# Kernel tuning notes

Hardware: AMD Instinct MI355X
Metric: run time of the kernel (lower is better)

Reference implementation:

```python
import jax, jax.numpy as jnp
import numpy as np
from jax import lax

T, N, F, H, E = 8, 20000, 128, 256, 320000
LEAK = 0.9


def setup_inputs() -> dict:
    key = jax.random.key(0)
    k = jax.random.split(key, 7)
    x = jax.random.normal(k[0], (T, N, F), dtype=jnp.float32)
    edge_index = jax.random.randint(k[1], (2, E), 0, N, dtype=jnp.int32)
    # reservoir weights, scaled ~1/sqrt(fan_in) so tanh stays in its active range
    w_in0 = jax.random.normal(k[2], (H, F), dtype=jnp.float32) / jnp.sqrt(F)
    w_rec0 = jax.random.normal(k[3], (H, H), dtype=jnp.float32) / jnp.sqrt(H)
    w_in1 = jax.random.normal(k[4], (H, H), dtype=jnp.float32) / jnp.sqrt(H)
    w_rec1 = jax.random.normal(k[5], (H, H), dtype=jnp.float32) / jnp.sqrt(H)
    leakage = jnp.array(LEAK, dtype=jnp.float32)
    return {"x": x, "edge_index": edge_index, "w_in0": w_in0, "w_rec0": w_rec0,
            "w_in1": w_in1, "w_rec1": w_rec1, "leakage": leakage}


def reference(x, edge_index, w_in0, w_rec0, w_in1, w_rec1, leakage):
    # DynamicGraphReservoir with 2 ReservoirConvLayers, fixed graph over time,
    # zero initial states, no pooling, fully=False, return_sequences=False.
    src, dst = edge_index[0], edge_index[1]
    num_nodes = x.shape[1]

    def layer(w_in, w_rec, inp, state):
        # neighbour aggregation: sum_{(j->i) in E} state[j]   (scatter-add)
        agg = jax.ops.segment_sum(state[src], dst, num_segments=num_nodes)
        return leakage * jnp.tanh(inp @ w_in.T + agg @ w_rec.T) + (1.0 - leakage) * state

    def step(states, xt):
        s0, s1 = states
        s0 = layer(w_in0, w_rec0, xt, s0)   # layer 0 consumes input signal
        s1 = layer(w_in1, w_rec1, s0, s1)   # layer 1 consumes layer-0 state
        return (s0, s1), None

    init = (jnp.zeros((num_nodes, w_rec0.shape[0]), x.dtype),
            jnp.zeros((num_nodes, w_rec1.shape[0]), x.dtype))
    (s0, s1), _ = lax.scan(step, init, x)
    return s1  # final-layer final state: (nodes, hidden)
```

## Files before the change

### kernel.cpp

```cpp
#include <hip/hip_runtime.h>
#include <math.h>

#define T_STEPS 8
#define N_NODES 20000
#define F_IN    128
#define H_DIM   256
#define E_EDGES 320000

typedef __attribute__((ext_vector_type(8))) short short8;
typedef __attribute__((ext_vector_type(4))) float f32x4;

__device__ __forceinline__ void split2(float v, unsigned short& h, unsigned short& l) {
    unsigned vi = __float_as_uint(v);
    h = (unsigned short)(vi >> 16);
    float hf = __uint_as_float(vi & 0xffff0000u);
    l = (unsigned short)(__float_as_uint(v - hf) >> 16);
}


__global__ void count_kernel(const int* __restrict__ dst, int* __restrict__ counts, int E) {
    int e = blockIdx.x * blockDim.x + threadIdx.x;
    if (e < E) atomicAdd(&counts[dst[e]], 1);
}

__global__ void scan_kernel(const int* __restrict__ counts, int* __restrict__ row_ptr,
                            int* __restrict__ cursors, int n) {
    __shared__ int buf[1024];
    __shared__ int carry_s;
    int tid = threadIdx.x;
    if (tid == 0) carry_s = 0;
    __syncthreads();
    for (int base = 0; base < n; base += 1024) {
        int i = base + tid;
        int v = (i < n) ? counts[i] : 0;
        buf[tid] = v;
        __syncthreads();
        for (int off = 1; off < 1024; off <<= 1) {
            int t = (tid >= off) ? buf[tid - off] : 0;
            __syncthreads();
            buf[tid] += t;
            __syncthreads();
        }
        int incl = buf[tid];
        int carry = carry_s;
        if (i < n) {
            int ex = carry + incl - v;
            row_ptr[i] = ex;
            cursors[i] = ex;
        }
        __syncthreads();
        if (tid == 1023) carry_s = carry + incl;
        __syncthreads();
    }
    if (tid == 0) row_ptr[n] = carry_s;
}

__global__ void fill_kernel(const int* __restrict__ src, const int* __restrict__ dst,
                            int* __restrict__ cursors, int* __restrict__ col, int E) {
    int e = blockIdx.x * blockDim.x + threadIdx.x;
    if (e < E) {
        int d = dst[e];
        int p = atomicAdd(&cursors[d], 1);
        col[p] = src[e];
    }
}


__global__ void cvt_frag(const float* __restrict__ W, int K,
                         unsigned short* __restrict__ fh, unsigned short* __restrict__ fl) {
    int g = blockIdx.x * 256 + threadIdx.x;
    int KP32 = K >> 5;
    int total = (H_DIM / 16) * KP32 * 64;
    if (g >= total) return;
    int lane = g & 63;
    int kp = (g >> 6) % KP32;
    int rt = g / (KP32 << 6);
    int r = rt * 16 + (lane & 15);
    int c = kp * 32 + (lane >> 4) * 8;
    const float* p = W + (size_t)r * K + c;
    short8 h, l;
    #pragma unroll
    for (int j = 0; j < 8; ++j) {
        unsigned short hh, ll;
        split2(p[j], hh, ll);
        h[j] = (short)hh; l[j] = (short)ll;
    }
    *(short8*)(fh + (size_t)g * 8) = h;
    *(short8*)(fl + (size_t)g * 8) = l;
}


__global__ __launch_bounds__(256) void fused_update(
        const float* __restrict__ A1, int K1,
        const float* __restrict__ s_prev,
        const unsigned short* __restrict__ B1h, const unsigned short* __restrict__ B1l,
        const unsigned short* __restrict__ B2h, const unsigned short* __restrict__ B2l,
        float* __restrict__ s_new,
        const int* __restrict__ row_ptr, const int* __restrict__ col,
        const float* __restrict__ leak_ptr, int do_gather) {
    __shared__ float aggs[32][260];
    const int tid = threadIdx.x;
    const int lane = tid & 63, w = tid >> 6;
    const int fr = lane & 15, fq = lane >> 4;
    const int m0 = blockIdx.x * 32;
    const int wn = w * 64;
    const int rtbase = w * 4;

    if (do_gather) {
        const float4* s4 = (const float4*)s_prev;
        #pragma unroll 1
        for (int i = 0; i < 8; ++i) {
            int r = w * 8 + i;
            int beg = row_ptr[m0 + r], end = row_ptr[m0 + r + 1];
            float4 a0 = {0,0,0,0}, a1 = {0,0,0,0}, a2 = {0,0,0,0}, a3 = {0,0,0,0};
            float4 a4 = {0,0,0,0}, a5 = {0,0,0,0}, a6 = {0,0,0,0}, a7 = {0,0,0,0};
            int j = beg;
            for (; j + 7 < end; j += 8) {
                float4 v0 = s4[(size_t)col[j    ] * 64 + lane];
                float4 v1 = s4[(size_t)col[j + 1] * 64 + lane];
                float4 v2 = s4[(size_t)col[j + 2] * 64 + lane];
                float4 v3 = s4[(size_t)col[j + 3] * 64 + lane];
                float4 v4 = s4[(size_t)col[j + 4] * 64 + lane];
                float4 v5 = s4[(size_t)col[j + 5] * 64 + lane];
                float4 v6 = s4[(size_t)col[j + 6] * 64 + lane];
                float4 v7 = s4[(size_t)col[j + 7] * 64 + lane];
                a0.x += v0.x; a0.y += v0.y; a0.z += v0.z; a0.w += v0.w;
                a1.x += v1.x; a1.y += v1.y; a1.z += v1.z; a1.w += v1.w;
                a2.x += v2.x; a2.y += v2.y; a2.z += v2.z; a2.w += v2.w;
                a3.x += v3.x; a3.y += v3.y; a3.z += v3.z; a3.w += v3.w;
                a4.x += v4.x; a4.y += v4.y; a4.z += v4.z; a4.w += v4.w;
                a5.x += v5.x; a5.y += v5.y; a5.z += v5.z; a5.w += v5.w;
                a6.x += v6.x; a6.y += v6.y; a6.z += v6.z; a6.w += v6.w;
                a7.x += v7.x; a7.y += v7.y; a7.z += v7.z; a7.w += v7.w;
            }
            for (; j + 3 < end; j += 4) {
                float4 v0 = s4[(size_t)col[j    ] * 64 + lane];
                float4 v1 = s4[(size_t)col[j + 1] * 64 + lane];
                float4 v2 = s4[(size_t)col[j + 2] * 64 + lane];
                float4 v3 = s4[(size_t)col[j + 3] * 64 + lane];
                a0.x += v0.x; a0.y += v0.y; a0.z += v0.z; a0.w += v0.w;
                a1.x += v1.x; a1.y += v1.y; a1.z += v1.z; a1.w += v1.w;
                a2.x += v2.x; a2.y += v2.y; a2.z += v2.z; a2.w += v2.w;
                a3.x += v3.x; a3.y += v3.y; a3.z += v3.z; a3.w += v3.w;
            }
            for (; j < end; ++j) {
                float4 v = s4[(size_t)col[j] * 64 + lane];
                a0.x += v.x; a0.y += v.y; a0.z += v.z; a0.w += v.w;
            }
            float4 t;
            t.x = ((a0.x + a1.x) + (a2.x + a3.x)) + ((a4.x + a5.x) + (a6.x + a7.x));
            t.y = ((a0.y + a1.y) + (a2.y + a3.y)) + ((a4.y + a5.y) + (a6.y + a7.y));
            t.z = ((a0.z + a1.z) + (a2.z + a3.z)) + ((a4.z + a5.z) + (a6.z + a7.z));
            t.w = ((a0.w + a1.w) + (a2.w + a3.w)) + ((a4.w + a5.w) + (a6.w + a7.w));
            *(float4*)&aggs[r][lane * 4] = t;
        }
    }

    f32x4 acc[2][4];
    #pragma unroll
    for (int mi = 0; mi < 2; ++mi)
        #pragma unroll
        for (int nt = 0; nt < 4; ++nt)
            acc[mi][nt] = (f32x4){0.f, 0.f, 0.f, 0.f};

    {
        const int KP32 = K1 >> 5;
        #pragma unroll 1
        for (int kp = 0; kp < KP32; ++kp) {
            short8 ah[2], al[2];
            #pragma unroll
            for (int mi = 0; mi < 2; ++mi) {
                const float* ap = A1 + (size_t)(m0 + mi * 16 + fr) * K1 + kp * 32 + fq * 8;
                float4 v0 = *(const float4*)ap;
                float4 v1 = *(const float4*)(ap + 4);
                unsigned short h, l;
                split2(v0.x, h, l); ah[mi][0] = (short)h; al[mi][0] = (short)l;
                split2(v0.y, h, l); ah[mi][1] = (short)h; al[mi][1] = (short)l;
                split2(v0.z, h, l); ah[mi][2] = (short)h; al[mi][2] = (short)l;
                split2(v0.w, h, l); ah[mi][3] = (short)h; al[mi][3] = (short)l;
                split2(v1.x, h, l); ah[mi][4] = (short)h; al[mi][4] = (short)l;
                split2(v1.y, h, l); ah[mi][5] = (short)h; al[mi][5] = (short)l;
                split2(v1.z, h, l); ah[mi][6] = (short)h; al[mi][6] = (short)l;
                split2(v1.w, h, l); ah[mi][7] = (short)h; al[mi][7] = (short)l;
            }
            short8 bh[4], bl[4];
            #pragma unroll
            for (int nt = 0; nt < 4; ++nt) {
                size_t off = ((size_t)((rtbase + nt) * KP32 + kp) * 64 + lane) * 8;
                bh[nt] = *(const short8*)(B1h + off);
                bl[nt] = *(const short8*)(B1l + off);
            }
            #pragma unroll
            for (int mi = 0; mi < 2; ++mi)
                #pragma unroll
                for (int nt = 0; nt < 4; ++nt) {
                    f32x4 c = acc[mi][nt];
                    c = __builtin_amdgcn_mfma_f32_16x16x32_bf16(ah[mi], bh[nt], c, 0, 0, 0);
                    c = __builtin_amdgcn_mfma_f32_16x16x32_bf16(al[mi], bh[nt], c, 0, 0, 0);
                    c = __builtin_amdgcn_mfma_f32_16x16x32_bf16(ah[mi], bl[nt], c, 0, 0, 0);
                    acc[mi][nt] = c;
                }
        }
    }

    if (B2h) {
        __syncthreads();
        #pragma unroll 1
        for (int kp = 0; kp < 8; ++kp) {
            short8 ah[2], al[2];
            #pragma unroll
            for (int mi = 0; mi < 2; ++mi) {
                const float* ap = &aggs[mi * 16 + fr][kp * 32 + fq * 8];
                float4 v0 = *(const float4*)ap;
                float4 v1 = *(const float4*)(ap + 4);
                unsigned short h, l;
                split2(v0.x, h, l); ah[mi][0] = (short)h; al[mi][0] = (short)l;
                split2(v0.y, h, l); ah[mi][1] = (short)h; al[mi][1] = (short)l;
                split2(v0.z, h, l); ah[mi][2] = (short)h; al[mi][2] = (short)l;
                split2(v0.w, h, l); ah[mi][3] = (short)h; al[mi][3] = (short)l;
                split2(v1.x, h, l); ah[mi][4] = (short)h; al[mi][4] = (short)l;
                split2(v1.y, h, l); ah[mi][5] = (short)h; al[mi][5] = (short)l;
                split2(v1.z, h, l); ah[mi][6] = (short)h; al[mi][6] = (short)l;
                split2(v1.w, h, l); ah[mi][7] = (short)h; al[mi][7] = (short)l;
            }
            short8 bh[4], bl[4];
            #pragma unroll
            for (int nt = 0; nt < 4; ++nt) {
                size_t off = ((size_t)((rtbase + nt) * 8 + kp) * 64 + lane) * 8;
                bh[nt] = *(const short8*)(B2h + off);
                bl[nt] = *(const short8*)(B2l + off);
            }
            #pragma unroll
            for (int mi = 0; mi < 2; ++mi)
                #pragma unroll
                for (int nt = 0; nt < 4; ++nt) {
                    f32x4 c = acc[mi][nt];
                    c = __builtin_amdgcn_mfma_f32_16x16x32_bf16(ah[mi], bh[nt], c, 0, 0, 0);
                    c = __builtin_amdgcn_mfma_f32_16x16x32_bf16(al[mi], bh[nt], c, 0, 0, 0);
                    c = __builtin_amdgcn_mfma_f32_16x16x32_bf16(ah[mi], bl[nt], c, 0, 0, 0);
                    acc[mi][nt] = c;
                }
        }
    }

    const float leak = leak_ptr[0], il = 1.0f - leak;
    #pragma unroll
    for (int mi = 0; mi < 2; ++mi)
        #pragma unroll
        for (int r = 0; r < 4; ++r) {
            int m = m0 + mi * 16 + fq * 4 + r;
            #pragma unroll
            for (int nt = 0; nt < 4; ++nt) {
                int n = wn + nt * 16 + fr;
                size_t idx = (size_t)m * H_DIM + n;
                float old = s_prev[idx];
                float pre = acc[mi][nt][r];
                float e = __expf(2.0f * pre);
                float th = 1.0f - 2.0f / (e + 1.0f);
                s_new[idx] = leak * th + il * old;
            }
        }
}


extern "C" void kernel_launch(void* const* d_in, const int* in_sizes, int n_in,
                              void* d_out, int out_size, void* d_ws, size_t ws_size,
                              hipStream_t stream) {
    const float* x        = (const float*)d_in[0];
    const int*   edge     = (const int*)d_in[1];
    const float* w_in0    = (const float*)d_in[2];
    const float* w_rec0   = (const float*)d_in[3];
    const float* w_in1    = (const float*)d_in[4];
    const float* w_rec1   = (const float*)d_in[5];
    const float* leak_ptr = (const float*)d_in[6];

    const int* src = edge;
    const int* dst = edge + E_EDGES;

    char* ws = (char*)d_ws;
    size_t off = 0;
    auto alloc = [&](size_t bytes) -> char* {
        char* p = ws + off;
        off += (bytes + 255) & ~(size_t)255;
        return p;
    };
    const size_t state_bytes = (size_t)N_NODES * H_DIM * sizeof(float);
    float* s0b[2]; float* s1b[2];
    s0b[0] = (float*)alloc(state_bytes);
    s0b[1] = (float*)alloc(state_bytes);
    s1b[0] = (float*)d_out;
    s1b[1] = (float*)alloc(state_bytes);
    unsigned short* w0h  = (unsigned short*)alloc(256 * 128 * 2);
    unsigned short* w0l  = (unsigned short*)alloc(256 * 128 * 2);
    unsigned short* wr0h = (unsigned short*)alloc(256 * 256 * 2);
    unsigned short* wr0l = (unsigned short*)alloc(256 * 256 * 2);
    unsigned short* w1h  = (unsigned short*)alloc(256 * 256 * 2);
    unsigned short* w1l  = (unsigned short*)alloc(256 * 256 * 2);
    unsigned short* wr1h = (unsigned short*)alloc(256 * 256 * 2);
    unsigned short* wr1l = (unsigned short*)alloc(256 * 256 * 2);
    int* row_ptr = (int*)alloc((N_NODES + 1) * sizeof(int));
    int* cursors = (int*)alloc(N_NODES * sizeof(int));
    int* counts  = (int*)alloc(N_NODES * sizeof(int));
    int* col     = (int*)alloc((size_t)E_EDGES * sizeof(int));

    hipMemsetAsync(s0b[0], 0, state_bytes, stream);
    hipMemsetAsync(s1b[0], 0, state_bytes, stream);
    hipMemsetAsync(counts, 0, N_NODES * sizeof(int), stream);

    cvt_frag<<<16, 256, 0, stream>>>(w_in0, F_IN, w0h, w0l);
    cvt_frag<<<32, 256, 0, stream>>>(w_rec0, H_DIM, wr0h, wr0l);
    cvt_frag<<<32, 256, 0, stream>>>(w_in1, H_DIM, w1h, w1l);
    cvt_frag<<<32, 256, 0, stream>>>(w_rec1, H_DIM, wr1h, wr1l);

    count_kernel<<<(E_EDGES + 255) / 256, 256, 0, stream>>>(dst, counts, E_EDGES);
    scan_kernel<<<1, 1024, 0, stream>>>(counts, row_ptr, cursors, N_NODES);
    fill_kernel<<<(E_EDGES + 255) / 256, 256, 0, stream>>>(src, dst, cursors, col, E_EDGES);

    dim3 ugrid(N_NODES / 32);

    for (int t = 0; t < T_STEPS; ++t) {
        const float* xt = x + (size_t)t * N_NODES * F_IN;
        int rd = t & 1, wr = rd ^ 1;
        int dg = (t > 0) ? 1 : 0;
        fused_update<<<ugrid, 256, 0, stream>>>(
            xt, F_IN, s0b[rd],
            w0h, w0l, dg ? wr0h : nullptr, dg ? wr0l : nullptr,
            s0b[wr], row_ptr, col, leak_ptr, dg);
        fused_update<<<ugrid, 256, 0, stream>>>(
            s0b[wr], H_DIM, s1b[rd],
            w1h, w1l, dg ? wr1h : nullptr, dg ? wr1l : nullptr,
            s1b[wr], row_ptr, col, leak_ptr, dg);
    }
}
```

Baseline: 1.172 ms.

## Skew layer-1 step t with layer-0 step t+1 into one merged launch

Layer 1 at step t and layer 0 at step t+1 both read only s0 at step t, so they are independent. This change runs them in a single kernel whose blocks alternate between the two tasks, which halves the launches in the time loop and doubles the blocks per launch. The aim is to cut launch overhead and tail idle time while keeping the per-block work unchanged. The risk is in the buffer ping-pong indexing across the skewed schedule, and in two working sets competing for cache at once.

```diff
diff --git a/kernel.cpp b/kernel.cpp
--- a/kernel.cpp
+++ b/kernel.cpp
@@ -90,19 +90,18 @@
 }
 
 
-__global__ __launch_bounds__(256) void fused_update(
+__device__ __forceinline__ void update_body(
         const float* __restrict__ A1, int K1,
         const float* __restrict__ s_prev,
         const unsigned short* __restrict__ B1h, const unsigned short* __restrict__ B1l,
         const unsigned short* __restrict__ B2h, const unsigned short* __restrict__ B2l,
         float* __restrict__ s_new,
         const int* __restrict__ row_ptr, const int* __restrict__ col,
-        const float* __restrict__ leak_ptr, int do_gather) {
-    __shared__ float aggs[32][260];
+        const float* __restrict__ leak_ptr, int do_gather,
+        int m0, float (*aggs)[260]) {
     const int tid = threadIdx.x;
     const int lane = tid & 63, w = tid >> 6;
     const int fr = lane & 15, fq = lane >> 4;
-    const int m0 = blockIdx.x * 32;
     const int wn = w * 64;
     const int rtbase = w * 4;
 
@@ -263,6 +262,48 @@
 }
 
 
+__global__ __launch_bounds__(256) void fused_update(
+        const float* __restrict__ A1, int K1,
+        const float* __restrict__ s_prev,
+        const unsigned short* __restrict__ B1h, const unsigned short* __restrict__ B1l,
+        const unsigned short* __restrict__ B2h, const unsigned short* __restrict__ B2l,
+        float* __restrict__ s_new,
+        const int* __restrict__ row_ptr, const int* __restrict__ col,
+        const float* __restrict__ leak_ptr, int do_gather) {
+    __shared__ float aggs[32][260];
+    update_body(A1, K1, s_prev, B1h, B1l, B2h, B2l, s_new,
+                row_ptr, col, leak_ptr, do_gather, blockIdx.x * 32, aggs);
+}
+
+
+__global__ __launch_bounds__(256) void fused_update2(
+        const float* __restrict__ A1a, int K1a, const float* __restrict__ spa,
+        const unsigned short* __restrict__ B1ha, const unsigned short* __restrict__ B1la,
+        const unsigned short* __restrict__ B2ha, const unsigned short* __restrict__ B2la,
+        float* __restrict__ sna, int dga,
+        const float* __restrict__ A1b, int K1b, const float* __restrict__ spb,
+        const unsigned short* __restrict__ B1hb, const unsigned short* __restrict__ B1lb,
+        const unsigned short* __restrict__ B2hb, const unsigned short* __restrict__ B2lb,
+        float* __restrict__ snb, int dgb,
+        const int* __restrict__ row_ptr, const int* __restrict__ col,
+        const float* __restrict__ leak_ptr) {
+    __shared__ float aggs[32][260];
+    const int task = blockIdx.x & 1;
+    const int m0 = (blockIdx.x >> 1) * 32;
+    const float* A1 = task ? A1b : A1a;
+    const int K1 = task ? K1b : K1a;
+    const float* sp = task ? spb : spa;
+    const unsigned short* B1h = task ? B1hb : B1ha;
+    const unsigned short* B1l = task ? B1lb : B1la;
+    const unsigned short* B2h = task ? B2hb : B2ha;
+    const unsigned short* B2l = task ? B2lb : B2la;
+    float* sn = task ? snb : sna;
+    const int dg = task ? dgb : dga;
+    update_body(A1, K1, sp, B1h, B1l, B2h, B2l, sn,
+                row_ptr, col, leak_ptr, dg, m0, aggs);
+}
+
+
 extern "C" void kernel_launch(void* const* d_in, const int* in_sizes, int n_in,
                               void* d_out, int out_size, void* d_ws, size_t ws_size,
                               hipStream_t stream) {
@@ -317,18 +358,33 @@
     fill_kernel<<<(E_EDGES + 255) / 256, 256, 0, stream>>>(src, dst, cursors, col, E_EDGES);
 
     dim3 ugrid(N_NODES / 32);
-
-    for (int t = 0; t < T_STEPS; ++t) {
-        const float* xt = x + (size_t)t * N_NODES * F_IN;
-        int rd = t & 1, wr = rd ^ 1;
-        int dg = (t > 0) ? 1 : 0;
-        fused_update<<<ugrid, 256, 0, stream>>>(
-            xt, F_IN, s0b[rd],
-            w0h, w0l, dg ? wr0h : nullptr, dg ? wr0l : nullptr,
-            s0b[wr], row_ptr, col, leak_ptr, dg);
-        fused_update<<<ugrid, 256, 0, stream>>>(
-            s0b[wr], H_DIM, s1b[rd],
-            w1h, w1l, dg ? wr1h : nullptr, dg ? wr1l : nullptr,
-            s1b[wr], row_ptr, col, leak_ptr, dg);
-    }
-}
+    dim3 ugrid2(2 * (N_NODES / 32));
+
+
+    fused_update<<<ugrid, 256, 0, stream>>>(
+        x, F_IN, s0b[0],
+        w0h, w0l, nullptr, nullptr,
+        s0b[1], row_ptr, col, leak_ptr, 0);
+
+    for (int m = 0; m < 7; ++m) {
+        const float* s0_cur = s0b[(m + 1) & 1];
+        float* s0_next      = s0b[m & 1];
+        const float* s1_rd  = s1b[m & 1];
+        float* s1_wr        = s1b[(m + 1) & 1];
+        const float* xt = x + (size_t)(m + 1) * N_NODES * F_IN;
+        int dg1 = (m > 0) ? 1 : 0;
+        fused_update2<<<ugrid2, 256, 0, stream>>>(
+            s0_cur, H_DIM, s1_rd,
+            w1h, w1l, dg1 ? wr1h : nullptr, dg1 ? wr1l : nullptr,
+            s1_wr, dg1,
+            xt, F_IN, s0_cur,
+            w0h, w0l, wr0h, wr0l,
+            s0_next, 1,
+            row_ptr, col, leak_ptr);
+    }
+
+    fused_update<<<ugrid, 256, 0, stream>>>(
+        s0b[0], H_DIM, s1b[1],
+        w1h, w1l, wr1h, wr1l,
+        s1b[0], row_ptr, col, leak_ptr, 1);
+}
```

Result: no change. 1.192 ms (+1.7%).

## Decouple neighbour gather from GEMM update and co-schedule it with the next layer

Applied to the files above, without the earlier changes.

Each state's neighbour aggregation now runs as a separate set of blocks in the kernel that produces the state's consumer-independent work. The aggregate is written to a global AGG buffer, so gather for the next layer overlaps with the current layer's GEMM update in one launch. The gather is re-split into 8 column chunks per 32-row group, with 8 lanes per edge slot and shuffle reductions. Column indices shrink to 16-bit. This trades the shared-memory aggregate and per-block serial gather for extra global traffic (writing and re-reading AGG) in exchange for better parallelism and overlap.

```diff
diff --git a/kernel.cpp b/kernel.cpp
--- a/kernel.cpp
+++ b/kernel.cpp
@@ -6,6 +6,9 @@
 #define F_IN    128
 #define H_DIM   256
 #define E_EDGES 320000
+
+#define G_UPD    625
+#define G_GATHER 5000
 
 typedef __attribute__((ext_vector_type(8))) short short8;
 typedef __attribute__((ext_vector_type(4))) float f32x4;
@@ -56,12 +59,12 @@
 }
 
 __global__ void fill_kernel(const int* __restrict__ src, const int* __restrict__ dst,
-                            int* __restrict__ cursors, int* __restrict__ col, int E) {
+                            int* __restrict__ cursors, unsigned short* __restrict__ col, int E) {
     int e = blockIdx.x * blockDim.x + threadIdx.x;
     if (e < E) {
         int d = dst[e];
         int p = atomicAdd(&cursors[d], 1);
-        col[p] = src[e];
+        col[p] = (unsigned short)src[e];
     }
 }
 
@@ -90,71 +93,62 @@
 }
 
 
-__global__ __launch_bounds__(256) void fused_update(
+__global__ __launch_bounds__(256) void step_kernel(
         const float* __restrict__ A1, int K1,
         const float* __restrict__ s_prev,
         const unsigned short* __restrict__ B1h, const unsigned short* __restrict__ B1l,
         const unsigned short* __restrict__ B2h, const unsigned short* __restrict__ B2l,
+        const float* __restrict__ AGGu,
         float* __restrict__ s_new,
-        const int* __restrict__ row_ptr, const int* __restrict__ col,
-        const float* __restrict__ leak_ptr, int do_gather) {
-    __shared__ float aggs[32][260];
+        const float* __restrict__ gsrc, float* __restrict__ gout, int do_gather,
+        const int* __restrict__ row_ptr, const unsigned short* __restrict__ col,
+        const float* __restrict__ leak_ptr) {
     const int tid = threadIdx.x;
     const int lane = tid & 63, w = tid >> 6;
+    const int upd_base = do_gather ? G_GATHER : 0;
+
+    if (blockIdx.x < (unsigned)upd_base) {
+        const int g = blockIdx.x;
+        const int chunk = g & 7;
+        const int nb = g >> 3;
+        const int slot = lane >> 3, comp = lane & 7;
+        const float4* src4 = (const float4*)gsrc + (size_t)chunk * 8 + comp;
+        #pragma unroll 1
+        for (int i = 0; i < 8; ++i) {
+            int r = nb * 32 + w * 8 + i;
+            int beg = row_ptr[r], end = row_ptr[r + 1];
+            float4 a = {0.f, 0.f, 0.f, 0.f};
+            int j = beg + slot;
+            for (; j + 8 < end; j += 16) {
+                int i0 = col[j];
+                int i1 = col[j + 8];
+                float4 v0 = src4[(size_t)i0 * 64];
+                float4 v1 = src4[(size_t)i1 * 64];
+                a.x += v0.x; a.y += v0.y; a.z += v0.z; a.w += v0.w;
+                a.x += v1.x; a.y += v1.y; a.z += v1.z; a.w += v1.w;
+            }
+            if (j < end) {
+                int i0 = col[j];
+                float4 v0 = src4[(size_t)i0 * 64];
+                a.x += v0.x; a.y += v0.y; a.z += v0.z; a.w += v0.w;
+            }
+            #pragma unroll
+            for (int m = 8; m < 64; m <<= 1) {
+                a.x += __shfl_xor(a.x, m);
+                a.y += __shfl_xor(a.y, m);
+                a.z += __shfl_xor(a.z, m);
+                a.w += __shfl_xor(a.w, m);
+            }
+            if (slot == 0)
+                *(float4*)(gout + (size_t)r * 256 + chunk * 32 + comp * 4) = a;
+        }
+        return;
+    }
+
+    const int m0 = (blockIdx.x - upd_base) * 32;
     const int fr = lane & 15, fq = lane >> 4;
-    const int m0 = blockIdx.x * 32;
     const int wn = w * 64;
     const int rtbase = w * 4;
-
-    if (do_gather) {
-        const float4* s4 = (const float4*)s_prev;
-        #pragma unroll 1
-        for (int i = 0; i < 8; ++i) {
-            int r = w * 8 + i;
-            int beg = row_ptr[m0 + r], end = row_ptr[m0 + r + 1];
-            float4 a0 = {0,0,0,0}, a1 = {0,0,0,0}, a2 = {0,0,0,0}, a3 = {0,0,0,0};
-            float4 a4 = {0,0,0,0}, a5 = {0,0,0,0}, a6 = {0,0,0,0}, a7 = {0,0,0,0};
-            int j = beg;
-            for (; j + 7 < end; j += 8) {
-                float4 v0 = s4[(size_t)col[j    ] * 64 + lane];
-                float4 v1 = s4[(size_t)col[j + 1] * 64 + lane];
-                float4 v2 = s4[(size_t)col[j + 2] * 64 + lane];
-                float4 v3 = s4[(size_t)col[j + 3] * 64 + lane];
-                float4 v4 = s4[(size_t)col[j + 4] * 64 + lane];
-                float4 v5 = s4[(size_t)col[j + 5] * 64 + lane];
-                float4 v6 = s4[(size_t)col[j + 6] * 64 + lane];
-                float4 v7 = s4[(size_t)col[j + 7] * 64 + lane];
-                a0.x += v0.x; a0.y += v0.y; a0.z += v0.z; a0.w += v0.w;
-                a1.x += v1.x; a1.y += v1.y; a1.z += v1.z; a1.w += v1.w;
-                a2.x += v2.x; a2.y += v2.y; a2.z += v2.z; a2.w += v2.w;
-                a3.x += v3.x; a3.y += v3.y; a3.z += v3.z; a3.w += v3.w;
-                a4.x += v4.x; a4.y += v4.y; a4.z += v4.z; a4.w += v4.w;
-                a5.x += v5.x; a5.y += v5.y; a5.z += v5.z; a5.w += v5.w;
-                a6.x += v6.x; a6.y += v6.y; a6.z += v6.z; a6.w += v6.w;
-                a7.x += v7.x; a7.y += v7.y; a7.z += v7.z; a7.w += v7.w;
-            }
-            for (; j + 3 < end; j += 4) {
-                float4 v0 = s4[(size_t)col[j    ] * 64 + lane];
-                float4 v1 = s4[(size_t)col[j + 1] * 64 + lane];
-                float4 v2 = s4[(size_t)col[j + 2] * 64 + lane];
-                float4 v3 = s4[(size_t)col[j + 3] * 64 + lane];
-                a0.x += v0.x; a0.y += v0.y; a0.z += v0.z; a0.w += v0.w;
-                a1.x += v1.x; a1.y += v1.y; a1.z += v1.z; a1.w += v1.w;
-                a2.x += v2.x; a2.y += v2.y; a2.z += v2.z; a2.w += v2.w;
-                a3.x += v3.x; a3.y += v3.y; a3.z += v3.z; a3.w += v3.w;
-            }
-            for (; j < end; ++j) {
-                float4 v = s4[(size_t)col[j] * 64 + lane];
-                a0.x += v.x; a0.y += v.y; a0.z += v.z; a0.w += v.w;
-            }
-            float4 t;
-            t.x = ((a0.x + a1.x) + (a2.x + a3.x)) + ((a4.x + a5.x) + (a6.x + a7.x));
-            t.y = ((a0.y + a1.y) + (a2.y + a3.y)) + ((a4.y + a5.y) + (a6.y + a7.y));
-            t.z = ((a0.z + a1.z) + (a2.z + a3.z)) + ((a4.z + a5.z) + (a6.z + a7.z));
-            t.w = ((a0.w + a1.w) + (a2.w + a3.w)) + ((a4.w + a5.w) + (a6.w + a7.w));
-            *(float4*)&aggs[r][lane * 4] = t;
-        }
-    }
 
     f32x4 acc[2][4];
     #pragma unroll
@@ -204,13 +198,12 @@
     }
 
     if (B2h) {
-        __syncthreads();
         #pragma unroll 1
         for (int kp = 0; kp < 8; ++kp) {
             short8 ah[2], al[2];
             #pragma unroll
             for (int mi = 0; mi < 2; ++mi) {
-                const float* ap = &aggs[mi * 16 + fr][kp * 32 + fq * 8];
+                const float* ap = AGGu + (size_t)(m0 + mi * 16 + fr) * H_DIM + kp * 32 + fq * 8;
                 float4 v0 = *(const float4*)ap;
                 float4 v1 = *(const float4*)(ap + 4);
                 unsigned short h, l;
@@ -290,6 +283,8 @@
     s0b[1] = (float*)alloc(state_bytes);
     s1b[0] = (float*)d_out;
     s1b[1] = (float*)alloc(state_bytes);
+    float* AGG0 = (float*)alloc(state_bytes);
+    float* AGG1 = (float*)alloc(state_bytes);
     unsigned short* w0h  = (unsigned short*)alloc(256 * 128 * 2);
     unsigned short* w0l  = (unsigned short*)alloc(256 * 128 * 2);
     unsigned short* wr0h = (unsigned short*)alloc(256 * 256 * 2);
@@ -301,7 +296,7 @@
     int* row_ptr = (int*)alloc((N_NODES + 1) * sizeof(int));
     int* cursors = (int*)alloc(N_NODES * sizeof(int));
     int* counts  = (int*)alloc(N_NODES * sizeof(int));
-    int* col     = (int*)alloc((size_t)E_EDGES * sizeof(int));
+    unsigned short* col = (unsigned short*)alloc((size_t)E_EDGES * sizeof(unsigned short));
 
     hipMemsetAsync(s0b[0], 0, state_bytes, stream);
     hipMemsetAsync(s1b[0], 0, state_bytes, stream);
@@ -316,19 +311,36 @@
     scan_kernel<<<1, 1024, 0, stream>>>(counts, row_ptr, cursors, N_NODES);
     fill_kernel<<<(E_EDGES + 255) / 256, 256, 0, stream>>>(src, dst, cursors, col, E_EDGES);
 
-    dim3 ugrid(N_NODES / 32);
-
-    for (int t = 0; t < T_STEPS; ++t) {
+    dim3 g_small(G_UPD);
+    dim3 g_big(G_GATHER + G_UPD);
+
+
+    step_kernel<<<g_small, 256, 0, stream>>>(
+        x, F_IN, s0b[0], w0h, w0l, nullptr, nullptr, nullptr, s0b[1],
+        nullptr, nullptr, 0, row_ptr, col, leak_ptr);
+    step_kernel<<<g_big, 256, 0, stream>>>(
+        s0b[1], H_DIM, s1b[0], w1h, w1l, nullptr, nullptr, nullptr, s1b[1],
+        s0b[1], AGG0, 1, row_ptr, col, leak_ptr);
+
+    for (int t = 1; t < T_STEPS; ++t) {
+        const float* s0_prev = s0b[t & 1];
+        float* s0_cur        = s0b[(t + 1) & 1];
+        const float* s1_prev = s1b[t & 1];
+        float* s1_cur        = s1b[(t + 1) & 1];
         const float* xt = x + (size_t)t * N_NODES * F_IN;
-        int rd = t & 1, wr = rd ^ 1;
-        int dg = (t > 0) ? 1 : 0;
-        fused_update<<<ugrid, 256, 0, stream>>>(
-            xt, F_IN, s0b[rd],
-            w0h, w0l, dg ? wr0h : nullptr, dg ? wr0l : nullptr,
-            s0b[wr], row_ptr, col, leak_ptr, dg);
-        fused_update<<<ugrid, 256, 0, stream>>>(
-            s0b[wr], H_DIM, s1b[rd],
-            w1h, w1l, dg ? wr1h : nullptr, dg ? wr1l : nullptr,
-            s1b[wr], row_ptr, col, leak_ptr, dg);
-    }
-}
+
+        step_kernel<<<g_big, 256, 0, stream>>>(
+            xt, F_IN, s0_prev, w0h, w0l, wr0h, wr0l, AGG0, s0_cur,
+            s1_prev, AGG1, 1, row_ptr, col, leak_ptr);
+
+        if (t < T_STEPS - 1) {
+            step_kernel<<<g_big, 256, 0, stream>>>(
+                s0_cur, H_DIM, s1_prev, w1h, w1l, wr1h, wr1l, AGG1, s1_cur,
+                s0_cur, AGG0, 1, row_ptr, col, leak_ptr);
+        } else {
+            step_kernel<<<g_small, 256, 0, stream>>>(
+                s0_cur, H_DIM, s1_prev, w1h, w1l, wr1h, wr1l, AGG1, s1_cur,
+                nullptr, nullptr, 0, row_ptr, col, leak_ptr);
+        }
+    }
+}
```

Result: slower. 1.665 ms (+42.0%).
